# Kernel optimization log

Measured on AMD Instinct MI355X. Metric: run time of the kernel, lower is better.

The kernel has to match this reference:

```python
import jax, jax.numpy as jnp
import numpy as np

T, H = 4096, 2048

def setup_inputs() -> dict:
    key = jax.random.key(0)
    k1, k2, k3 = jax.random.split(key, 3)
    x_sequence = jax.random.normal(k1, (T, H), dtype=jnp.float32)
    lamda = jax.random.normal(k2, (H,), dtype=jnp.float32) * 0.2
    B = jax.random.normal(k3, (H, H), dtype=jnp.float32) / jnp.sqrt(jnp.float32(H))
    return {"x_sequence": x_sequence, "lamda": lamda, "B": B}

def reference(x_sequence, lamda, B):
    # h_t = lamda \odot h_{t-1} + B @ x_t ; initial h_0 = 0 (reset_rtrl_state).
    # Returns stacked h over all T steps, matching torch.stack(outputs).
    def step(h, x_t):
        h_next = lamda * h + B @ x_t  # [H]
        return h_next, h_next
    h0 = jnp.zeros_like(lamda)
    _, hs = jax.lax.scan(step, h0, x_sequence)  # hs: [T, H]
    return hs
```

## Files before the change

### kernel.cpp

```cpp
#include <hip/hip_runtime.h>
#include <hip/hip_bf16.h>

#define T_DIM 4096
#define H_DIM 2048
#define K_DIM 2048
#define NCHUNK 64
#define CLEN 64

typedef float f32x4 __attribute__((ext_vector_type(4)));
typedef _Float16 f16x8 __attribute__((ext_vector_type(8)));

typedef const __attribute__((address_space(1))) char* gp1;
typedef __attribute__((address_space(3))) char* lp3;

static const size_t nX = (size_t)T_DIM * K_DIM;
static const size_t nB = (size_t)H_DIM * K_DIM;

__global__ __launch_bounds__(256) void cvt_swz_all(const float* __restrict__ X,
                                                   const float* __restrict__ Bm,
                                                   _Float16* __restrict__ Xh,
                                                   _Float16* __restrict__ Bh) {
    size_t i = ((size_t)blockIdx.x * 256 + threadIdx.x) * 8;
    const float* in;
    _Float16* out;
    size_t j;
    if (i < nX) { in = X;  out = Xh; j = i; }
    else        { in = Bm; out = Bh; j = i - nX; }
    int row  = (int)(j >> 11);
    int colB = (int)(j & 2047) * 2;
    float a[8];
    *(f32x4*)(a)     = *(const f32x4*)(in + j);
    *(f32x4*)(a + 4) = *(const f32x4*)(in + j + 4);
    f16x8 h;
#pragma unroll
    for (int k = 0; k < 8; ++k) h[k] = (_Float16)a[k];
    size_t ob = (size_t)row * 4096 + (size_t)(colB ^ ((row & 7) << 4));
    *(f16x8*)((char*)out + ob) = h;
}

__global__ __launch_bounds__(256) void gemm_f16(const _Float16* __restrict__ Xh,
                                                const _Float16* __restrict__ Bh,
                                                float* __restrict__ Y) {
    __shared__ __align__(16) _Float16 sA[2][128 * 64];
    __shared__ __align__(16) _Float16 sB[2][128 * 64];

    int bid = blockIdx.x;
    int swz = (bid & 7) * 64 + (bid >> 3);
    const int h0 = (swz & 15) * 128;
    const int t0 = (swz >> 4) * 128;

    const int tid  = threadIdx.x;
    const int lane = tid & 63;
    const int wave = tid >> 6;
    const int wrow = wave >> 1;
    const int wcol = wave & 1;
    const int ln15 = lane & 15;
    const int kq   = lane >> 4;

    f32x4 acc[4][4] = {};

    const int srow = tid >> 3;
    const int kcB  = (tid & 7) * 16;
    size_t gA0[4], gB0[4];
    unsigned ldsOff[4];
#pragma unroll
    for (int t = 0; t < 4; ++t) {
        gA0[t] = (size_t)(t0 + srow + t * 32) * 4096 + kcB;
        gB0[t] = (size_t)(h0 + srow + t * 32) * 4096 + kcB;
        ldsOff[t] = (unsigned)((t * 256 + wave * 64) * 16);
    }

    int baseA[4], swzA[4], baseB[4], swzB[4];
#pragma unroll
    for (int m = 0; m < 4; ++m) {
        int rA = wrow * 64 + m * 16 + ln15;
        baseA[m] = rA * 128; swzA[m] = (rA & 7) << 4;
        int rB = wcol * 64 + m * 16 + ln15;
        baseB[m] = rB * 128; swzB[m] = (rB & 7) << 4;
    }

#define STAGE(buf, kt)                                                                   \
    {                                                                                    \
        _Pragma("unroll")                                                                \
        for (int t = 0; t < 4; ++t) {                                                    \
            __builtin_amdgcn_global_load_lds((gp1)((const char*)Xh + gA0[t] + (kt) * 128), \
                                             (lp3)((char*)sA[buf] + ldsOff[t]), 16, 0, 0); \
            __builtin_amdgcn_global_load_lds((gp1)((const char*)Bh + gB0[t] + (kt) * 128), \
                                             (lp3)((char*)sB[buf] + ldsOff[t]), 16, 0, 0); \
        }                                                                                \
    }

    STAGE(0, 0);
    __syncthreads();

    int cur = 0;
    for (int kt = 0; kt < K_DIM / 64; ++kt) {
        if (kt + 1 < K_DIM / 64) STAGE(cur ^ 1, kt + 1);
        const char* pA = (const char*)sA[cur];
        const char* pB = (const char*)sB[cur];
#pragma unroll
        for (int kk = 0; kk < 2; ++kk) {
            const int kb = kk * 64 + kq * 16;
            f16x8 fa[4], fb[4];
#pragma unroll
            for (int m = 0; m < 4; ++m)
                fa[m] = *(const f16x8*)(pA + baseA[m] + (kb ^ swzA[m]));
#pragma unroll
            for (int m = 0; m < 4; ++m)
                fb[m] = *(const f16x8*)(pB + baseB[m] + (kb ^ swzB[m]));
#pragma unroll
            for (int m = 0; m < 4; ++m)
#pragma unroll
                for (int n = 0; n < 4; ++n)
                    acc[m][n] = __builtin_amdgcn_mfma_f32_16x16x32_f16(fa[m], fb[n], acc[m][n], 0, 0, 0);
        }
        __syncthreads();
        cur ^= 1;
    }
#undef STAGE

#pragma unroll
    for (int m = 0; m < 4; ++m) {
        int row = t0 + wrow * 64 + m * 16 + kq * 4;
#pragma unroll
        for (int n = 0; n < 4; ++n) {
            int col = h0 + wcol * 64 + n * 16 + ln15;
#pragma unroll
            for (int j = 0; j < 4; ++j)
                Y[(size_t)(row + j) * H_DIM + col] = acc[m][n][j];
        }
    }
}

__global__ __launch_bounds__(256) void scanA(const float* __restrict__ Y,
                                             const float* __restrict__ lamda,
                                             float* __restrict__ e) {
    int c = blockIdx.x >> 3;
    int h = (blockIdx.x & 7) * 256 + threadIdx.x;
    float lam = lamda[h];
    float s = 0.f;
    const float* p = Y + (size_t)c * CLEN * H_DIM + h;
#pragma unroll
    for (int t = 0; t < CLEN; ++t) { s = fmaf(lam, s, *p); p += H_DIM; }
    e[(size_t)c * H_DIM + h] = s;
}

__global__ __launch_bounds__(256) void scanCB(float* __restrict__ Y,
                                              const float* __restrict__ lamda,
                                              const float* __restrict__ e) {
    int c = blockIdx.x >> 3;
    int h = (blockIdx.x & 7) * 256 + threadIdx.x;
    float lam = lamda[h];
    float lamL = lam;
#pragma unroll
    for (int i = 0; i < 6; ++i) lamL *= lamL;
    float s = 0.f;
    for (int ci = 0; ci < c; ++ci)
        s = fmaf(lamL, s, e[(size_t)ci * H_DIM + h]);
    float* q = Y + (size_t)c * CLEN * H_DIM + h;
#pragma unroll
    for (int t = 0; t < CLEN; ++t) {
        float v = fmaf(lam, s, q[(size_t)t * H_DIM]);
        q[(size_t)t * H_DIM] = v;
        s = v;
    }
}

__global__ __launch_bounds__(256) void gemm_xbT_split(const float* __restrict__ X,
                                                      const float* __restrict__ Bm,
                                                      float* __restrict__ Y) {
    __shared__ __align__(16) _Float16 Ah[128 * 64];
    __shared__ __align__(16) _Float16 Al[128 * 64];
    __shared__ __align__(16) _Float16 Bh2[128 * 64];
    __shared__ __align__(16) _Float16 Bl[128 * 64];

    const int tid  = threadIdx.x;
    const int t0   = blockIdx.y * 128;
    const int h0   = blockIdx.x * 128;
    const int lane = tid & 63;
    const int wave = tid >> 6;
    const int wrow = wave >> 1;
    const int wcol = wave & 1;
    const int ln15 = lane & 15;
    const int kq   = lane >> 4;

    f32x4 acc[4][4] = {};

    int baseA[4], swzA[4], baseB[4], swzB[4];
#pragma unroll
    for (int m = 0; m < 4; ++m) {
        int rA = wrow * 64 + m * 16 + ln15;
        baseA[m] = rA * 128; swzA[m] = (rA & 7) << 4;
        int rB = wcol * 64 + m * 16 + ln15;
        baseB[m] = rB * 128; swzB[m] = (rB & 7) << 4;
    }

    for (int kt = 0; kt < K_DIM / 64; ++kt) {
        const int k0 = kt * 64;
        __syncthreads();
#pragma unroll
        for (int t = 0; t < 4; ++t) {
            int c   = tid + t * 256;
            int row = c >> 3;
            int kc  = (c & 7) * 8;
            size_t gA = (size_t)(t0 + row) * K_DIM + k0 + kc;
            size_t gB = (size_t)(h0 + row) * K_DIM + k0 + kc;
            float a[8], b[8];
            *(float4*)(a)     = *(const float4*)(X + gA);
            *(float4*)(a + 4) = *(const float4*)(X + gA + 4);
            *(float4*)(b)     = *(const float4*)(Bm + gB);
            *(float4*)(b + 4) = *(const float4*)(Bm + gB + 4);
            f16x8 ah, al, bh, bl;
#pragma unroll
            for (int j = 0; j < 8; ++j) {
                _Float16 hh = (_Float16)a[j];
                ah[j] = hh; al[j] = (_Float16)(a[j] - (float)hh);
                _Float16 gg = (_Float16)b[j];
                bh[j] = gg; bl[j] = (_Float16)(b[j] - (float)gg);
            }
            int off = row * 128 + ((kc * 2) ^ ((row & 7) << 4));
            *(f16x8*)((char*)Ah + off)  = ah;
            *(f16x8*)((char*)Al + off)  = al;
            *(f16x8*)((char*)Bh2 + off) = bh;
            *(f16x8*)((char*)Bl + off)  = bl;
        }
        __syncthreads();
#pragma unroll
        for (int kk = 0; kk < 2; ++kk) {
            const int kb = kk * 64 + kq * 16;
            f16x8 fa[4], fb[4], ft[4];
#pragma unroll
            for (int m = 0; m < 4; ++m)
                fa[m] = *(const f16x8*)((const char*)Ah + baseA[m] + (kb ^ swzA[m]));
#pragma unroll
            for (int m = 0; m < 4; ++m)
                fb[m] = *(const f16x8*)((const char*)Bh2 + baseB[m] + (kb ^ swzB[m]));
#pragma unroll
            for (int m = 0; m < 4; ++m)
#pragma unroll
                for (int n = 0; n < 4; ++n)
                    acc[m][n] = __builtin_amdgcn_mfma_f32_16x16x32_f16(fa[m], fb[n], acc[m][n], 0, 0, 0);
#pragma unroll
            for (int m = 0; m < 4; ++m)
                ft[m] = *(const f16x8*)((const char*)Bl + baseB[m] + (kb ^ swzB[m]));
#pragma unroll
            for (int m = 0; m < 4; ++m)
#pragma unroll
                for (int n = 0; n < 4; ++n)
                    acc[m][n] = __builtin_amdgcn_mfma_f32_16x16x32_f16(fa[m], ft[n], acc[m][n], 0, 0, 0);
#pragma unroll
            for (int m = 0; m < 4; ++m)
                ft[m] = *(const f16x8*)((const char*)Al + baseA[m] + (kb ^ swzA[m]));
#pragma unroll
            for (int m = 0; m < 4; ++m)
#pragma unroll
                for (int n = 0; n < 4; ++n)
                    acc[m][n] = __builtin_amdgcn_mfma_f32_16x16x32_f16(ft[m], fb[n], acc[m][n], 0, 0, 0);
        }
    }

#pragma unroll
    for (int m = 0; m < 4; ++m) {
        int row = t0 + wrow * 64 + m * 16 + kq * 4;
#pragma unroll
        for (int n = 0; n < 4; ++n) {
            int col = h0 + wcol * 64 + n * 16 + ln15;
#pragma unroll
            for (int j = 0; j < 4; ++j)
                Y[(size_t)(row + j) * H_DIM + col] = acc[m][n][j];
        }
    }
}

extern "C" void kernel_launch(void* const* d_in, const int* in_sizes, int n_in,
                              void* d_out, int out_size, void* d_ws, size_t ws_size,
                              hipStream_t stream) {
    const float* X   = (const float*)d_in[0];
    const float* lam = (const float*)d_in[1];
    const float* Bm  = (const float*)d_in[2];
    float* Y = (float*)d_out;

    const size_t needFused = (nX + nB) * sizeof(_Float16)
                           + (size_t)NCHUNK * H_DIM * sizeof(float);

    if (ws_size >= needFused) {
        _Float16* Xh = (_Float16*)d_ws;
        _Float16* Bh = Xh + nX;
        float* e = (float*)(Bh + nB);

        int cvtBlocks = (int)((nX + nB) / 8 / 256);
        cvt_swz_all<<<dim3(cvtBlocks), 256, 0, stream>>>(X, Bm, Xh, Bh);
        gemm_f16<<<dim3(512), 256, 0, stream>>>(Xh, Bh, Y);
        scanA<<<dim3(NCHUNK * 8), 256, 0, stream>>>(Y, lam, e);
        scanCB<<<dim3(NCHUNK * 8), 256, 0, stream>>>(Y, lam, e);
    } else {
        dim3 grid(H_DIM / 128, T_DIM / 128);
        gemm_xbT_split<<<grid, 256, 0, stream>>>(X, Bm, Y);
        float* e = (float*)d_ws;
        scanA<<<dim3(NCHUNK * 8), 256, 0, stream>>>(Y, lam, e);
        scanCB<<<dim3(NCHUNK * 8), 256, 0, stream>>>(Y, lam, e);
    }
}
```

Baseline: 86.68 us.

## Fuse chunk-end scan reduction into GEMM epilogue and tighten pipeline barriers

Each GEMM block now computes the per-chunk decayed sum (the scanA result) directly from its MFMA accumulators. It weights rows by powers of lamda and reduces across lanes with shuffles, which removes the separate scanA kernel and its re-read of Y. The k-loop also replaces __syncthreads with explicit vmcnt/lgkmcnt waits and raw s_barrier calls so the next tile's loads overlap compute. The new waits depend on exact counts of outstanding loads, which is fragile, and the power-weighted summation order differs from the sequential scan.

```diff
diff --git a/kernel.cpp b/kernel.cpp
--- a/kernel.cpp
+++ b/kernel.cpp
@@ -6,6 +6,7 @@
 #define K_DIM 2048
 #define NCHUNK 64
 #define CLEN 64
+#define NT (K_DIM / 64)
 
 typedef float f32x4 __attribute__((ext_vector_type(4)));
 typedef _Float16 f16x8 __attribute__((ext_vector_type(8)));
@@ -40,7 +41,9 @@
 
 __global__ __launch_bounds__(256) void gemm_f16(const _Float16* __restrict__ Xh,
                                                 const _Float16* __restrict__ Bh,
-                                                float* __restrict__ Y) {
+                                                const float* __restrict__ lamda,
+                                                float* __restrict__ Y,
+                                                float* __restrict__ e) {
     __shared__ __align__(16) _Float16 sA[2][128 * 64];
     __shared__ __align__(16) _Float16 sB[2][128 * 64];
 
@@ -90,34 +93,51 @@
         }                                                                                \
     }
 
+#define COMPUTE(buf)                                                                     \
+    {                                                                                    \
+        const char* pA = (const char*)sA[buf];                                           \
+        const char* pB = (const char*)sB[buf];                                           \
+        _Pragma("unroll")                                                                \
+        for (int kk = 0; kk < 2; ++kk) {                                                 \
+            const int kb = kk * 64 + kq * 16;                                            \
+            f16x8 fa[4], fb[4];                                                          \
+            _Pragma("unroll")                                                            \
+            for (int m = 0; m < 4; ++m)                                                  \
+                fa[m] = *(const f16x8*)(pA + baseA[m] + (kb ^ swzA[m]));                 \
+            _Pragma("unroll")                                                            \
+            for (int m = 0; m < 4; ++m)                                                  \
+                fb[m] = *(const f16x8*)(pB + baseB[m] + (kb ^ swzB[m]));                 \
+            _Pragma("unroll")                                                            \
+            for (int m = 0; m < 4; ++m)                                                  \
+                _Pragma("unroll")                                                        \
+                for (int n = 0; n < 4; ++n)                                              \
+                    acc[m][n] = __builtin_amdgcn_mfma_f32_16x16x32_f16(fa[m], fb[n],     \
+                                                                      acc[m][n], 0, 0, 0); \
+        }                                                                                \
+    }
+
     STAGE(0, 0);
-    __syncthreads();
-
     int cur = 0;
-    for (int kt = 0; kt < K_DIM / 64; ++kt) {
-        if (kt + 1 < K_DIM / 64) STAGE(cur ^ 1, kt + 1);
-        const char* pA = (const char*)sA[cur];
-        const char* pB = (const char*)sB[cur];
-#pragma unroll
-        for (int kk = 0; kk < 2; ++kk) {
-            const int kb = kk * 64 + kq * 16;
-            f16x8 fa[4], fb[4];
-#pragma unroll
-            for (int m = 0; m < 4; ++m)
-                fa[m] = *(const f16x8*)(pA + baseA[m] + (kb ^ swzA[m]));
-#pragma unroll
-            for (int m = 0; m < 4; ++m)
-                fb[m] = *(const f16x8*)(pB + baseB[m] + (kb ^ swzB[m]));
-#pragma unroll
-            for (int m = 0; m < 4; ++m)
-#pragma unroll
-                for (int n = 0; n < 4; ++n)
-                    acc[m][n] = __builtin_amdgcn_mfma_f32_16x16x32_f16(fa[m], fb[n], acc[m][n], 0, 0, 0);
-        }
-        __syncthreads();
+    for (int kt = 0; kt < NT - 1; ++kt) {
+        STAGE(cur ^ 1, kt + 1);
+        asm volatile("s_waitcnt vmcnt(8)" ::: "memory");
+        __builtin_amdgcn_sched_barrier(0);
+        __builtin_amdgcn_s_barrier();
+        __builtin_amdgcn_sched_barrier(0);
+        COMPUTE(cur);
+        __builtin_amdgcn_sched_barrier(0);
+        asm volatile("s_waitcnt lgkmcnt(0)" ::: "memory");
+        __builtin_amdgcn_s_barrier();
+        __builtin_amdgcn_sched_barrier(0);
         cur ^= 1;
     }
+    asm volatile("s_waitcnt vmcnt(0)" ::: "memory");
+    __builtin_amdgcn_sched_barrier(0);
+    __builtin_amdgcn_s_barrier();
+    __builtin_amdgcn_sched_barrier(0);
+    COMPUTE(cur);
 #undef STAGE
+#undef COMPUTE
 
 #pragma unroll
     for (int m = 0; m < 4; ++m) {
@@ -130,19 +150,31 @@
                 Y[(size_t)(row + j) * H_DIM + col] = acc[m][n][j];
         }
     }
-}
-
-__global__ __launch_bounds__(256) void scanA(const float* __restrict__ Y,
-                                             const float* __restrict__ lamda,
-                                             float* __restrict__ e) {
-    int c = blockIdx.x >> 3;
-    int h = (blockIdx.x & 7) * 256 + threadIdx.x;
-    float lam = lamda[h];
-    float s = 0.f;
-    const float* p = Y + (size_t)c * CLEN * H_DIM + h;
-#pragma unroll
-    for (int t = 0; t < CLEN; ++t) { s = fmaf(lam, s, *p); p += H_DIM; }
-    e[(size_t)c * H_DIM + h] = s;
+
+    const int c = (t0 >> 6) + wrow;
+#pragma unroll
+    for (int n = 0; n < 4; ++n) {
+        int col = h0 + wcol * 64 + n * 16 + ln15;
+        float lam  = lamda[col];
+        float lam2 = lam * lam;
+        float lam4 = lam2 * lam2;
+        float lam16 = lam4 * lam4 * lam4 * lam4;
+        float hsum = 0.f;
+#pragma unroll
+        for (int m = 0; m < 4; ++m) {
+            float hm = fmaf(fmaf(fmaf(acc[m][n][0], lam, acc[m][n][1]), lam,
+                                 acc[m][n][2]), lam, acc[m][n][3]);
+            hsum = fmaf(hsum, lam16, hm);
+        }
+        float w = 1.f;
+        if (kq < 3) w = lam4;
+        if (kq < 2) w *= lam4;
+        if (kq < 1) w *= lam4;
+        float T = hsum * w;
+        T += __shfl_xor(T, 16);
+        T += __shfl_xor(T, 32);
+        if (kq == 0) e[(size_t)c * H_DIM + col] = T;
+    }
 }
 
 __global__ __launch_bounds__(256) void scanCB(float* __restrict__ Y,
@@ -195,7 +227,7 @@
         baseB[m] = rB * 128; swzB[m] = (rB & 7) << 4;
     }
 
-    for (int kt = 0; kt < K_DIM / 64; ++kt) {
+    for (int kt = 0; kt < NT; ++kt) {
         const int k0 = kt * 64;
         __syncthreads();
 #pragma unroll
@@ -272,6 +304,19 @@
     }
 }
 
+__global__ __launch_bounds__(256) void scanA(const float* __restrict__ Y,
+                                             const float* __restrict__ lamda,
+                                             float* __restrict__ e) {
+    int c = blockIdx.x >> 3;
+    int h = (blockIdx.x & 7) * 256 + threadIdx.x;
+    float lam = lamda[h];
+    float s = 0.f;
+    const float* p = Y + (size_t)c * CLEN * H_DIM + h;
+#pragma unroll
+    for (int t = 0; t < CLEN; ++t) { s = fmaf(lam, s, *p); p += H_DIM; }
+    e[(size_t)c * H_DIM + h] = s;
+}
+
 extern "C" void kernel_launch(void* const* d_in, const int* in_sizes, int n_in,
                               void* d_out, int out_size, void* d_ws, size_t ws_size,
                               hipStream_t stream) {
@@ -290,8 +335,7 @@
 
         int cvtBlocks = (int)((nX + nB) / 8 / 256);
         cvt_swz_all<<<dim3(cvtBlocks), 256, 0, stream>>>(X, Bm, Xh, Bh);
-        gemm_f16<<<dim3(512), 256, 0, stream>>>(Xh, Bh, Y);
-        scanA<<<dim3(NCHUNK * 8), 256, 0, stream>>>(Y, lam, e);
+        gemm_f16<<<dim3(512), 256, 0, stream>>>(Xh, Bh, lam, Y, e);
         scanCB<<<dim3(NCHUNK * 8), 256, 0, stream>>>(Y, lam, e);
     } else {
         dim3 grid(H_DIM / 128, T_DIM / 128);
```

Measured after the change: 81.91 us. -5.5%, faster.
